# Kernel tuning notes

Hardware: AMD Instinct MI355X
Metric: run time of the kernel (lower is better)

Reference implementation:

```python
import jax, jax.numpy as jnp
import numpy as np

HEADS = 4

def _conv1x1(x, w, b):
    # 1x1 conv == channel-mixing matmul; w: [C_out, C_in], b: [C_out]
    return jnp.einsum('bchw,oc->bohw', x, w) + b[None, :, None, None]

def setup_inputs() -> dict:
    key = jax.random.key(0)
    ks = jax.random.split(key, 9)
    B, C, H, W = 4, 64, 64, 64
    x = jax.random.normal(ks[0], (B, C, H, W), dtype=jnp.float32)
    scale = 0.05
    wq = jax.random.normal(ks[1], (C, C), dtype=jnp.float32) * scale
    bq = jax.random.normal(ks[2], (C,), dtype=jnp.float32) * scale
    wk = jax.random.normal(ks[3], (C, C), dtype=jnp.float32) * scale
    bk = jax.random.normal(ks[4], (C,), dtype=jnp.float32) * scale
    wv = jax.random.normal(ks[5], (C, C), dtype=jnp.float32) * scale
    bv = jax.random.normal(ks[6], (C,), dtype=jnp.float32) * scale
    wp = jax.random.normal(ks[7], (C, C), dtype=jnp.float32) * scale
    bp = jax.random.normal(ks[8], (C,), dtype=jnp.float32) * scale
    return {"x": x, "wq": wq, "bq": bq, "wk": wk, "bk": bk,
            "wv": wv, "bv": bv, "wp": wp, "bp": bp}

def reference(x, wq, bq, wk, bk, wv, bv, wp, bp):
    B, C, H, W = x.shape
    HW = H * W
    ch = C // HEADS  # head dim
    q = _conv1x1(x, wq, bq).reshape(B, HEADS, ch, HW)
    k = _conv1x1(x, wk, bk).reshape(B, HEADS, ch, HW)
    v = _conv1x1(x, wv, bv).reshape(B, HEADS, ch, HW)
    # scores[b,h,i,j] = sum_c q[b,h,c,i] * k[b,h,c,j]  -> [B, H, HW, HW]
    scores = jnp.einsum('bhci,bhcj->bhij', q, k)
    attn = jax.nn.softmax(scores, axis=-1)
    # out: [B, heads, HW, ch]
    out = jnp.einsum('bhij,bhcj->bhic', attn, v)
    # faithful to torch .view: raw contiguous reshape (NOT a transpose back)
    out = out.reshape(B, C, H, W)
    return _conv1x1(out, wp, bp)
```

## Files before the change

kernel.cpp:

```cpp
#include <hip/hip_runtime.h>

#define LOG2E 1.4426950408889634f


using s8v   = __attribute__((ext_vector_type(8))) short;
using u16x8 = __attribute__((ext_vector_type(8))) unsigned short;
using f32x4 = __attribute__((ext_vector_type(4))) float;

static __device__ __forceinline__ unsigned short bf16b(float f) {
  return __builtin_bit_cast(unsigned short, (__bf16)f);
}

__global__ __launch_bounds__(256) void qkv_proj(
    const float* __restrict__ x,
    const float* __restrict__ wq, const float* __restrict__ bq,
    const float* __restrict__ wk, const float* __restrict__ bk,
    const float* __restrict__ wv, const float* __restrict__ bv,
    float* __restrict__ qb, unsigned short* __restrict__ kT,
    unsigned short* __restrict__ vb) {
  __shared__ __align__(16) float xs[64][64];
  __shared__ float wqs[64][65];
  __shared__ float wks[64][65];
  __shared__ float wvs[64][65];
  int t = threadIdx.x;
  int b = blockIdx.x >> 6;
  int px0 = (blockIdx.x & 63) << 6;
#pragma unroll
  for (int kk = 0; kk < 16; kk++) {
    int idx = kk * 256 + t;
    int c = idx >> 6, px = idx & 63;
    xs[c][px] = x[((size_t)(b * 64 + c) << 12) + px0 + px];
    int o = idx >> 6, c2 = idx & 63;
    wqs[c2][o] = wq[idx];
    wks[c2][o] = wk[idx];
    wvs[c2][o] = wv[idx];
  }
  __syncthreads();

  int o = t & 63;
  int pw = (t >> 6) << 4;
  float aq[16], ak[16], av[16];
#pragma unroll
  for (int p = 0; p < 16; p++) { aq[p] = 0.f; ak[p] = 0.f; av[p] = 0.f; }

  for (int c = 0; c < 64; c++) {
    float wqv = wqs[c][o], wkv = wks[c][o], wvv = wvs[c][o];
    float xr[16];
#pragma unroll
    for (int g = 0; g < 4; g++) {
      float4 x4 = *reinterpret_cast<const float4*>(&xs[c][pw + 4 * g]);
      xr[4 * g] = x4.x; xr[4 * g + 1] = x4.y; xr[4 * g + 2] = x4.z; xr[4 * g + 3] = x4.w;
    }
#pragma unroll
    for (int p = 0; p < 16; p++) {
      aq[p] += wqv * xr[p];
      ak[p] += wkv * xr[p];
      av[p] += wvv * xr[p];
    }
  }

  float bqv = bq[o], bkv = bk[o], bvv = bv[o];
  {
    float* dstq = qb + ((size_t)(b * 64 + o) << 12) + px0 + pw;
#pragma unroll
    for (int g = 0; g < 4; g++) {
      float4 q4 = { (aq[4 * g + 0] + bqv) * LOG2E, (aq[4 * g + 1] + bqv) * LOG2E,
                    (aq[4 * g + 2] + bqv) * LOG2E, (aq[4 * g + 3] + bqv) * LOG2E };
      reinterpret_cast<float4*>(dstq)[g] = q4;
    }
    unsigned short* dstv = vb + ((size_t)(b * 64 + o) << 12) + px0 + pw;
    u16x8 v0, v1;
#pragma unroll
    for (int p = 0; p < 8; p++) {
      v0[p] = bf16b(av[p] + bvv);
      v1[p] = bf16b(av[8 + p] + bvv);
    }
    *reinterpret_cast<u16x8*>(dstv) = v0;
    *reinterpret_cast<u16x8*>(dstv + 8) = v1;
  }
  int bh = b * 4 + (o >> 4);
  int chn = o & 15;
  size_t kb = ((size_t)bh << 16) + ((size_t)(px0 + pw) << 4) + chn;
#pragma unroll
  for (int p = 0; p < 16; p++) {
    kT[kb + ((size_t)p << 4)] = bf16b(ak[p] + bkv);
  }
}

__global__ __launch_bounds__(256) void attn_mfma(
    const float* __restrict__ qb, const unsigned short* __restrict__ kT,
    const unsigned short* __restrict__ vb, float* __restrict__ ao) {
  __shared__ float red[4][64][18];
  const int tid  = threadIdx.x;
  const int w    = tid >> 6;
  const int lane = tid & 63;
  const int i_   = lane & 15;
  const int q4   = lane >> 4;
  const int chb  = (q4 & 1) << 3;

  const int orig = ((blockIdx.x & 7) << 7) + (blockIdx.x >> 3);
  const int bh = orig >> 6;
  const int i0 = (orig & 63) << 6;
  const int b = bh >> 2, h = bh & 3;

  s8v BQ[4];
#pragma unroll
  for (int g = 0; g < 4; ++g) {
    const float* qp = qb + (((size_t)(b * 64 + h * 16 + chb)) << 12) + (i0 + (g << 4) + i_);
#pragma unroll
    for (int e = 0; e < 8; ++e) {
      float f = qp[(size_t)e << 12];
      __bf16 hi = (__bf16)f;
      float v = (q4 < 2) ? (float)hi : (f - (float)hi);
      BQ[g][e] = __builtin_bit_cast(short, (__bf16)v);
    }
  }

  f32x4 acc[4];
  float l[4];
#pragma unroll
  for (int g = 0; g < 4; ++g) {
    acc[g] = (f32x4){0.f, 0.f, 0.f, 0.f};
    l[g] = 0.f;
  }

  const unsigned short* vpb = vb + (((size_t)(b * 64 + h * 16 + i_)) << 12);
  const unsigned short* kpb = kT + ((size_t)bh << 16);

  for (int t = 0; t < 32; ++t) {
    const int jb = (w << 10) + (t << 5);
    s8v AV;
    {
      struct { uint2 a, b; } pair;
      pair.a = *(const uint2*)(vpb + jb + (q4 << 2));
      pair.b = *(const uint2*)(vpb + jb + 16 + (q4 << 2));
      AV = __builtin_bit_cast(s8v, pair);
    }
    s8v AK0 = *(const s8v*)(kpb + (((size_t)(jb + i_)) << 4) + chb);
    s8v AK1 = *(const s8v*)(kpb + (((size_t)(jb + 16 + i_)) << 4) + chb);

#pragma unroll
    for (int g = 0; g < 4; ++g) {
      f32x4 z = {0.f, 0.f, 0.f, 0.f};
      f32x4 s0 = __builtin_amdgcn_mfma_f32_16x16x32_bf16(AK0, BQ[g], z, 0, 0, 0);
      f32x4 s1 = __builtin_amdgcn_mfma_f32_16x16x32_bf16(AK1, BQ[g], z, 0, 0, 0);
      float p0 = __builtin_amdgcn_exp2f(s0[0]);
      float p1 = __builtin_amdgcn_exp2f(s0[1]);
      float p2 = __builtin_amdgcn_exp2f(s0[2]);
      float p3 = __builtin_amdgcn_exp2f(s0[3]);
      float p4 = __builtin_amdgcn_exp2f(s1[0]);
      float p5 = __builtin_amdgcn_exp2f(s1[1]);
      float p6 = __builtin_amdgcn_exp2f(s1[2]);
      float p7 = __builtin_amdgcn_exp2f(s1[3]);
      l[g] += (((p0 + p1) + (p2 + p3)) + ((p4 + p5) + (p6 + p7)));
      s8v PB;
      PB[0] = (short)bf16b(p0); PB[1] = (short)bf16b(p1);
      PB[2] = (short)bf16b(p2); PB[3] = (short)bf16b(p3);
      PB[4] = (short)bf16b(p4); PB[5] = (short)bf16b(p5);
      PB[6] = (short)bf16b(p6); PB[7] = (short)bf16b(p7);
      acc[g] = __builtin_amdgcn_mfma_f32_16x16x32_bf16(AV, PB, acc[g], 0, 0, 0);
    }
  }

#pragma unroll
  for (int g = 0; g < 4; ++g) {
    float lg = l[g];
    lg += __shfl_xor(lg, 16);
    lg += __shfl_xor(lg, 32);
    int iq = (g << 4) + i_;
    if (q4 == 0) red[w][iq][0] = lg;
    red[w][iq][1 + (q4 << 2) + 0] = acc[g][0];
    red[w][iq][1 + (q4 << 2) + 1] = acc[g][1];
    red[w][iq][1 + (q4 << 2) + 2] = acc[g][2];
    red[w][iq][1 + (q4 << 2) + 3] = acc[g][3];
  }
  __syncthreads();

  {
    int iq = tid & 63, quad = tid >> 6;
    float L = (red[0][iq][0] + red[1][iq][0]) + (red[2][iq][0] + red[3][iq][0]);
    float o0 = 0.f, o1 = 0.f, o2 = 0.f, o3 = 0.f;
#pragma unroll
    for (int s = 0; s < 4; ++s) {
      o0 += red[s][iq][1 + (quad << 2) + 0];
      o1 += red[s][iq][1 + (quad << 2) + 1];
      o2 += red[s][iq][1 + (quad << 2) + 2];
      o3 += red[s][iq][1 + (quad << 2) + 3];
    }
    float inv = 1.0f / L;
    float4 o = { o0 * inv, o1 * inv, o2 * inv, o3 * inv };
    *(float4*)&ao[((((size_t)bh << 12) + i0 + iq) << 4) + (quad << 2)] = o;
  }
}

__global__ __launch_bounds__(256) void out_proj(
    const float* __restrict__ a, const float* __restrict__ wp,
    const float* __restrict__ bp, float* __restrict__ out) {
  __shared__ __align__(16) float as[64][64];
  __shared__ float wps[64][65];
  int t = threadIdx.x;
  int b = blockIdx.x >> 6;
  int px0 = (blockIdx.x & 63) << 6;
#pragma unroll
  for (int kk = 0; kk < 16; kk++) {
    int idx = kk * 256 + t;
    int c = idx >> 6, px = idx & 63;
    as[c][px] = a[((size_t)b << 18) + ((size_t)c << 12) + px0 + px];
    int o = idx >> 6, c2 = idx & 63;
    wps[c2][o] = wp[idx];
  }
  __syncthreads();

  int o = t & 63;
  int pw = (t >> 6) << 4;
  float acc[16];
#pragma unroll
  for (int p = 0; p < 16; p++) acc[p] = 0.f;
  for (int c = 0; c < 64; c++) {
    float wv = wps[c][o];
    float xr[16];
#pragma unroll
    for (int g = 0; g < 4; g++) {
      float4 x4 = *reinterpret_cast<const float4*>(&as[c][pw + 4 * g]);
      xr[4 * g] = x4.x; xr[4 * g + 1] = x4.y; xr[4 * g + 2] = x4.z; xr[4 * g + 3] = x4.w;
    }
#pragma unroll
    for (int p = 0; p < 16; p++) acc[p] += wv * xr[p];
  }
  float bv = bp[o];
  float* dst = out + ((size_t)(b * 64 + o) << 12) + px0 + pw;
#pragma unroll
  for (int g = 0; g < 4; g++) {
    float4 v4 = { acc[4 * g + 0] + bv, acc[4 * g + 1] + bv,
                  acc[4 * g + 2] + bv, acc[4 * g + 3] + bv };
    reinterpret_cast<float4*>(dst)[g] = v4;
  }
}

extern "C" void kernel_launch(void* const* d_in, const int* in_sizes, int n_in,
                              void* d_out, int out_size, void* d_ws, size_t ws_size,
                              hipStream_t stream) {
  (void)in_sizes; (void)n_in; (void)out_size; (void)ws_size;
  const float* x  = (const float*)d_in[0];
  const float* wq = (const float*)d_in[1];
  const float* bq = (const float*)d_in[2];
  const float* wk = (const float*)d_in[3];
  const float* bk = (const float*)d_in[4];
  const float* wv = (const float*)d_in[5];
  const float* bv = (const float*)d_in[6];
  const float* wp = (const float*)d_in[7];
  const float* bp = (const float*)d_in[8];

  float* ws = (float*)d_ws;
  float* qb = ws;
  unsigned short* kT = (unsigned short*)(ws + (1u << 20));
  unsigned short* vT = (unsigned short*)(ws + (1u << 20) + (1u << 19));
  float* ao = ws + 2u * (1u << 20);

  qkv_proj<<<256, 256, 0, stream>>>(x, wq, bq, wk, bk, wv, bv, qb, kT, vT);
  attn_mfma<<<1024, 256, 0, stream>>>(qb, kT, vT, ao);
  out_proj<<<256, 256, 0, stream>>>(ao, wp, bp, (float*)d_out);
}
```

Measured before the change: 71.83 us.

## Precompute bf16 hi/lo Q split in projection and use 8 waves per attention block

The QKV projection now writes Q as bf16 hi/lo halves in the same channel-contiguous layout as K, so the attention kernel loads each Q fragment with one 16-byte vector load. This replaces eight strided fp32 loads and a conversion per lane. The attention kernel also doubles its block to 512 threads, splitting the key range over 8 waves instead of 4, so each wave runs half as many iterations. In exchange the cross-wave reduction in shared memory gets larger, and occupancy depends on register pressure under the new launch bounds.

```diff
diff --git a/kernel.cpp b/kernel.cpp
--- a/kernel.cpp
+++ b/kernel.cpp
@@ -16,7 +16,7 @@
     const float* __restrict__ wq, const float* __restrict__ bq,
     const float* __restrict__ wk, const float* __restrict__ bk,
     const float* __restrict__ wv, const float* __restrict__ bv,
-    float* __restrict__ qb, unsigned short* __restrict__ kT,
+    unsigned short* __restrict__ qsplit, unsigned short* __restrict__ kT,
     unsigned short* __restrict__ vb) {
   __shared__ __align__(16) float xs[64][64];
   __shared__ float wqs[64][65];
@@ -61,13 +61,6 @@
 
   float bqv = bq[o], bkv = bk[o], bvv = bv[o];
   {
-    float* dstq = qb + ((size_t)(b * 64 + o) << 12) + px0 + pw;
-#pragma unroll
-    for (int g = 0; g < 4; g++) {
-      float4 q4 = { (aq[4 * g + 0] + bqv) * LOG2E, (aq[4 * g + 1] + bqv) * LOG2E,
-                    (aq[4 * g + 2] + bqv) * LOG2E, (aq[4 * g + 3] + bqv) * LOG2E };
-      reinterpret_cast<float4*>(dstq)[g] = q4;
-    }
     unsigned short* dstv = vb + ((size_t)(b * 64 + o) << 12) + px0 + pw;
     u16x8 v0, v1;
 #pragma unroll
@@ -83,14 +76,19 @@
   size_t kb = ((size_t)bh << 16) + ((size_t)(px0 + pw) << 4) + chn;
 #pragma unroll
   for (int p = 0; p < 16; p++) {
+    float f = (aq[p] + bqv) * LOG2E;
+    __bf16 hi = (__bf16)f;
+    qsplit[kb + ((size_t)p << 4)] = __builtin_bit_cast(unsigned short, hi);
+    qsplit[kb + ((size_t)p << 4) + (1u << 20)] = bf16b(f - (float)hi);
     kT[kb + ((size_t)p << 4)] = bf16b(ak[p] + bkv);
   }
 }
 
-__global__ __launch_bounds__(256) void attn_mfma(
-    const float* __restrict__ qb, const unsigned short* __restrict__ kT,
+__global__ __launch_bounds__(512, 8) void attn_mfma(
+    const unsigned short* __restrict__ qsplit,
+    const unsigned short* __restrict__ kT,
     const unsigned short* __restrict__ vb, float* __restrict__ ao) {
-  __shared__ float red[4][64][18];
+  __shared__ float red[8][64][18];
   const int tid  = threadIdx.x;
   const int w    = tid >> 6;
   const int lane = tid & 63;
@@ -103,17 +101,12 @@
   const int i0 = (orig & 63) << 6;
   const int b = bh >> 2, h = bh & 3;
 
+  const unsigned short* qpb =
+      qsplit + ((size_t)(q4 >> 1) << 20) + ((size_t)bh << 16) + chb;
   s8v BQ[4];
 #pragma unroll
   for (int g = 0; g < 4; ++g) {
-    const float* qp = qb + (((size_t)(b * 64 + h * 16 + chb)) << 12) + (i0 + (g << 4) + i_);
-#pragma unroll
-    for (int e = 0; e < 8; ++e) {
-      float f = qp[(size_t)e << 12];
-      __bf16 hi = (__bf16)f;
-      float v = (q4 < 2) ? (float)hi : (f - (float)hi);
-      BQ[g][e] = __builtin_bit_cast(short, (__bf16)v);
-    }
+    BQ[g] = *(const s8v*)(qpb + ((size_t)(i0 + (g << 4) + i_) << 4));
   }
 
   f32x4 acc[4];
@@ -127,8 +120,8 @@
   const unsigned short* vpb = vb + (((size_t)(b * 64 + h * 16 + i_)) << 12);
   const unsigned short* kpb = kT + ((size_t)bh << 16);
 
-  for (int t = 0; t < 32; ++t) {
-    const int jb = (w << 10) + (t << 5);
+  for (int t = 0; t < 16; ++t) {
+    const int jb = (w << 9) + (t << 5);
     s8v AV;
     {
       struct { uint2 a, b; } pair;
@@ -176,12 +169,12 @@
   }
   __syncthreads();
 
-  {
+  if (tid < 256) {
     int iq = tid & 63, quad = tid >> 6;
-    float L = (red[0][iq][0] + red[1][iq][0]) + (red[2][iq][0] + red[3][iq][0]);
-    float o0 = 0.f, o1 = 0.f, o2 = 0.f, o3 = 0.f;
-#pragma unroll
-    for (int s = 0; s < 4; ++s) {
+    float L = 0.f, o0 = 0.f, o1 = 0.f, o2 = 0.f, o3 = 0.f;
+#pragma unroll
+    for (int s = 0; s < 8; ++s) {
+      L  += red[s][iq][0];
       o0 += red[s][iq][1 + (quad << 2) + 0];
       o1 += red[s][iq][1 + (quad << 2) + 1];
       o2 += red[s][iq][1 + (quad << 2) + 2];
@@ -251,13 +244,13 @@
   const float* wp = (const float*)d_in[7];
   const float* bp = (const float*)d_in[8];
 
-  float* ws = (float*)d_ws;
-  float* qb = ws;
-  unsigned short* kT = (unsigned short*)(ws + (1u << 20));
-  unsigned short* vT = (unsigned short*)(ws + (1u << 20) + (1u << 19));
-  float* ao = ws + 2u * (1u << 20);
-
-  qkv_proj<<<256, 256, 0, stream>>>(x, wq, bq, wk, bk, wv, bv, qb, kT, vT);
-  attn_mfma<<<1024, 256, 0, stream>>>(qb, kT, vT, ao);
+  char* ws = (char*)d_ws;
+  unsigned short* qsplit = (unsigned short*)ws;
+  unsigned short* kT = (unsigned short*)(ws + (4u << 20));
+  unsigned short* vT = (unsigned short*)(ws + (6u << 20));
+  float* ao = (float*)(ws + (8u << 20));
+
+  qkv_proj<<<256, 256, 0, stream>>>(x, wq, bq, wk, bk, wv, bv, qsplit, kT, vT);
+  attn_mfma<<<1024, 512, 0, stream>>>(qsplit, kT, vT, ao);
   out_proj<<<256, 256, 0, stream>>>(ao, wp, bp, (float*)d_out);
 }
```

Result: slower. 115.5 us (+60.8%).
